# Optimization experiments

Measured on AMD Instinct MI355X. Metric: run time of the kernel, lower is better.

## Reference

```python
import jax, jax.numpy as jnp
import numpy as np

B, S, H, E = 32, 4096, 512, 512

def setup_inputs() -> dict:
    key = jax.random.key(0)
    ks = jax.random.split(key, 11)
    sc = 1.0 / np.sqrt(H)
    return {
        "context": jax.random.normal(ks[0], (B, S, H), jnp.float32),
        "h": jax.random.normal(ks[1], (B, H), jnp.float32),
        "x": jax.random.normal(ks[2], (B, E), jnp.float32),
        "We": jax.random.normal(ks[3], (H, H), jnp.float32) * sc,
        "be": jax.random.normal(ks[4], (H,), jnp.float32) * sc,
        "Wd": jax.random.normal(ks[5], (H, H), jnp.float32) * sc,
        "bd": jax.random.normal(ks[6], (H,), jnp.float32) * sc,
        "Wv": jax.random.normal(ks[7], (H,), jnp.float32) * sc,
        "bv": jax.random.normal(ks[8], (1,), jnp.float32) * sc,
        "Wr": jax.random.normal(ks[9], (2 * H, 2 * H + E), jnp.float32) * (1.0 / np.sqrt(2 * H + E)),
        "br": jax.random.normal(ks[10], (2 * H,), jnp.float32) * sc,
    }

def reference(context, h, x, We, be, Wd, bd, Wv, bv, Wr, br):
    # gamma_encoder: [B,S,H]; gamma_decoder: [B,1,H]
    ge = jnp.einsum('bsh,kh->bsk', context, We) + be
    gd = h @ Wd.T + bd
    # additive scores -> [B,S]
    scores = jnp.einsum('bsh,h->bs', jnp.tanh(ge + gd[:, None, :]), Wv) + bv[0]
    weights = jax.nn.softmax(scores, axis=1)
    # context vector c_t: [B,H]
    c_t = jnp.einsum('bs,bsh->bh', weights, context)
    # linear_r on [c_t, h, x] -> [B,2H]
    r_t = jnp.concatenate([c_t, h, x], axis=1) @ Wr.T + br
    # maxout over pairs: view [B,H,2].max(-1)
    output = jnp.max(r_t.reshape(-1, r_t.shape[1] // 2, 2), axis=2)
    return (output, weights)
```

## Files before the change

### kernel.cpp

```cpp
#include <hip/hip_runtime.h>

typedef __attribute__((ext_vector_type(8))) short bf16x8;
typedef __attribute__((ext_vector_type(16))) float f32x16;

typedef __attribute__((address_space(3))) unsigned int lds_u32;
typedef __attribute__((address_space(1))) unsigned int glb_u32;

__device__ inline unsigned int cvt_pk_bf16(float lo, float hi){
  unsigned int r;
  asm("v_cvt_pk_bf16_f32 %0, %1, %2" : "=v"(r) : "v"(lo), "v"(hi));
  return r;
}
__device__ inline bf16x8 pack8(float4 a, float4 b){
  union { unsigned int u[4]; bf16x8 v; } r;
  r.u[0]=cvt_pk_bf16(a.x,a.y); r.u[1]=cvt_pk_bf16(a.z,a.w);
  r.u[2]=cvt_pk_bf16(b.x,b.y); r.u[3]=cvt_pk_bf16(b.z,b.w);
  return r.v;
}
__device__ inline float fast_tanh(float x){
  float e = __builtin_amdgcn_exp2f(x * 2.8853900817779268f);
  return 1.0f - 2.0f * __builtin_amdgcn_rcpf(e + 1.0f);
}
#define LOG2E 1.4426950408889634f

__global__ __launch_bounds__(256) void we_conv(const float* __restrict__ We,
                                               uint4* __restrict__ weFrag){
  int gid = blockIdx.x * 256 + threadIdx.x;
  int l  = gid & 63;
  int hc = gid >> 10;
  int colv = (hc >> 1)*32 + (l & 31);
  int k = ((hc & 1) << 8) + ((gid >> 6) & 15)*16 + (l >> 5)*8;
  const float4* src = (const float4*)(We + colv*512 + k);
  float4 f0 = src[0], f1 = src[1];
  weFrag[gid] = make_uint4(cvt_pk_bf16(f0.x,f0.y), cvt_pk_bf16(f0.z,f0.w),
                           cvt_pk_bf16(f1.x,f1.y), cvt_pk_bf16(f1.z,f1.w));
}

__global__ __launch_bounds__(256) void gd_kernel(const float* __restrict__ hvec,
                                                 const float* __restrict__ Wd,
                                                 const float* __restrict__ bd,
                                                 const float* __restrict__ be,
                                                 float* __restrict__ gd){
  __shared__ float hs[512];
  int b = blockIdx.x >> 2, kc = blockIdx.x & 3;
  int tid = threadIdx.x;
  hs[tid]       = hvec[b*512 + tid];
  hs[tid + 256] = hvec[b*512 + 256 + tid];
  __syncthreads();
  int k  = kc*128 + (tid >> 1);
  int hh = (tid & 1) * 256;
  const float4* wrow = (const float4*)(Wd + (size_t)k*512 + hh);
  const float4* hv4  = (const float4*)(hs + hh);
  float acc = 0.f;
  #pragma unroll 8
  for (int i = 0; i < 64; ++i){
    float4 w = wrow[i]; float4 u = hv4[i];
    acc += w.x*u.x + w.y*u.y + w.z*u.z + w.w*u.w;
  }
  acc += __shfl_xor(acc, 1);
  if ((tid & 1) == 0) gd[b*512 + k] = acc + bd[k] + be[k];
}

__global__ __launch_bounds__(256, 2) void score_kernel(
    const float* __restrict__ ctx, const char* __restrict__ weFrag,
    const float* __restrict__ gd, const float* __restrict__ Wv,
    float* __restrict__ scores, unsigned int* __restrict__ ctp,
    float* __restrict__ MS){
  __shared__ char lds[3*16384 + 4096];
  float* gdwv = (float*)(lds + 49152);

  const int tid  = threadIdx.x;
  const int wid  = tid >> 6;
  const int lane = tid & 63;
  const int bid  = blockIdx.x;
  const int row0 = bid * 128;
  const int b    = bid >> 5;
  const int col  = lane & 31;
  const int hi   = lane >> 5;

  if (tid < 128) ((float4*)gdwv)[tid] = ((const float4*)(gd + b*512))[tid];
  else           ((float4*)gdwv)[tid] = ((const float4*)Wv)[tid - 128];

  bf16x8 afrag[32];
  {
    const float4* ap = (const float4*)(ctx + (size_t)(row0 + wid*32 + col)*512 + hi*8);
    #pragma unroll
    for (int t = 0; t < 32; ++t)
      afrag[t] = pack8(ap[t*4], ap[t*4 + 1]);
  }

  asm volatile("s_waitcnt lgkmcnt(0)" ::: "memory");

  #define ISSUE(HC, BUF) do { \
    const char* _g = weFrag + ((size_t)(HC))*16384 + wid*4096; \
    char* _l = lds + (BUF)*16384 + wid*4096; \
    _Pragma("unroll") \
    for (int _i = 0; _i < 4; ++_i) \
      __builtin_amdgcn_global_load_lds((const glb_u32*)(_g + _i*1024 + lane*16), \
                                       (lds_u32*)(_l + _i*1024), 16, 0, 0); \
  } while(0)

  ISSUE(0, 0);
  ISSUE(1, 1);

  f32x16 acc;
  float sc[16];
  #pragma unroll
  for (int r = 0; r < 16; ++r) sc[r] = 0.f;

  for (int nc = 0; nc < 16; ++nc){
    const int hc0 = 2*nc, hc1 = 2*nc + 1;

    asm volatile("s_waitcnt vmcnt(4)" ::: "memory");
    __builtin_amdgcn_s_barrier();
    if (hc0 < 30) ISSUE(hc0 + 2, (hc0 + 2) % 3);
    {
      const char* bb = lds + (hc0 % 3)*16384 + lane*16;
      #pragma unroll
      for (int r = 0; r < 16; ++r) acc[r] = 0.f;
      __builtin_amdgcn_s_setprio(1);
      #pragma unroll
      for (int t = 0; t < 16; ++t){
        bf16x8 bf = *(const bf16x8*)(bb + t*1024);
        acc = __builtin_amdgcn_mfma_f32_32x32x16_bf16(afrag[t], bf, acc, 0, 0, 0);
      }
      __builtin_amdgcn_s_setprio(0);
    }

    if (nc < 15) asm volatile("s_waitcnt vmcnt(4)" ::: "memory");
    else         asm volatile("s_waitcnt vmcnt(0)" ::: "memory");
    __builtin_amdgcn_s_barrier();
    if (hc1 < 30) ISSUE(hc1 + 2, (hc1 + 2) % 3);
    {
      const char* bb = lds + (hc1 % 3)*16384 + lane*16;
      __builtin_amdgcn_s_setprio(1);
      #pragma unroll
      for (int t = 0; t < 16; ++t){
        bf16x8 bf = *(const bf16x8*)(bb + t*1024);
        acc = __builtin_amdgcn_mfma_f32_32x32x16_bf16(afrag[16 + t], bf, acc, 0, 0, 0);
      }
      __builtin_amdgcn_s_setprio(0);
    }

    {
      float gdv = gdwv[nc*32 + col];
      float wvv = gdwv[512 + nc*32 + col];
      #pragma unroll
      for (int r = 0; r < 16; ++r)
        sc[r] += fast_tanh(acc[r] + gdv) * wvv;
    }
  }
  #undef ISSUE

  #pragma unroll
  for (int r = 0; r < 16; ++r){
    #pragma unroll
    for (int m = 1; m <= 16; m <<= 1) sc[r] += __shfl_xor(sc[r], m);
  }

  float* scl  = gdwv;
  float* wl   = gdwv + 128;
  float* redp = gdwv + 256;
  __syncthreads();

  if (col == 0){
    int rbase = wid*32 + 4*hi;
    float* so = scores + row0 + rbase;
    #pragma unroll
    for (int r = 0; r < 16; ++r){
      int rr = (r & 3) + 8*(r >> 2);
      so[rr] = sc[r];
      scl[rbase + rr] = sc[r];
    }
  }
  __syncthreads();

  float M = -1e30f;
  {
    const float4* s4 = (const float4*)scl;
    #pragma unroll
    for (int i = 0; i < 32; ++i){
      float4 v = s4[i];
      M = fmaxf(M, fmaxf(fmaxf(v.x, v.y), fmaxf(v.z, v.w)));
    }
  }
  if (tid < 128){
    float w = __builtin_amdgcn_exp2f((scl[tid] - M) * LOG2E);
    wl[tid] = w;
    #pragma unroll
    for (int o = 1; o < 64; o <<= 1) w += __shfl_xor(w, o);
    if ((tid & 63) == 0) redp[tid >> 6] = w;
  }
  __syncthreads();
  float S_blk = redp[0] + redp[1];

  float cA = 0.f, cB = 0.f;
  #pragma unroll
  for (int p = 0; p < 4; ++p){
    if (wid == p){
      int rl = col;
      char* dst = lds + rl*1024;
      int swz = (rl & 7) << 4;
      #pragma unroll
      for (int t = 0; t < 32; ++t){
        union { bf16x8 v; uint4 q; } u; u.v = afrag[t];
        *(uint4*)(dst + ((t*32 + hi*16) ^ swz)) = u.q;
      }
    }
    __syncthreads();
    const float* wp = wl + p*32;
    #pragma unroll 8
    for (int r = 0; r < 32; ++r){
      unsigned int u = *(const unsigned int*)(lds + r*1024 + ((tid*4) ^ ((r & 7) << 4)));
      float cw = wp[r];
      union { unsigned int q; float f; } flo, fhi;
      flo.q = u << 16;
      fhi.q = u & 0xffff0000u;
      cA += cw * flo.f;
      cB += cw * fhi.f;
    }
    __syncthreads();
  }
  ctp[(size_t)bid*256 + tid] = cvt_pk_bf16(cA, cB);
  if (tid == 0){ MS[2*bid] = M; MS[2*bid + 1] = S_blk; }
}

__global__ __launch_bounds__(256) void combine_kernel(const unsigned int* __restrict__ ctp,
                                                      const float* __restrict__ MS,
                                                      float* __restrict__ ct,
                                                      float* __restrict__ mbuf){
  __shared__ float wsh[32];
  __shared__ float msh[2];
  int b = blockIdx.x, tid = threadIdx.x;
  if (tid < 32){
    float Mi = MS[(b*32 + tid)*2];
    float Si = MS[(b*32 + tid)*2 + 1];
    float M = Mi;
    #pragma unroll
    for (int o = 1; o < 32; o <<= 1) M = fmaxf(M, __shfl_xor(M, o));
    float w = __builtin_amdgcn_exp2f((Mi - M) * LOG2E);
    float d = w * Si;
    #pragma unroll
    for (int o = 1; o < 32; o <<= 1) d += __shfl_xor(d, o);
    wsh[tid] = w;
    if (tid == 0){ msh[0] = M; msh[1] = 1.0f / d; }
  }
  __syncthreads();
  float invd = msh[1];
  float a0 = 0.f, a1 = 0.f;
  #pragma unroll 8
  for (int i = 0; i < 32; ++i){
    unsigned int u = ctp[(size_t)(b*32 + i)*256 + tid];
    float w = wsh[i];
    union { unsigned int q; float f; } flo, fhi;
    flo.q = u << 16;
    fhi.q = u & 0xffff0000u;
    a0 += w * flo.f;
    a1 += w * fhi.f;
  }
  ((float2*)(ct + b*512))[tid] = make_float2(a0 * invd, a1 * invd);
  if (tid == 0){ mbuf[2*b] = msh[0]; mbuf[2*b + 1] = invd; }
}

__global__ __launch_bounds__(256) void weights_kernel(const float* __restrict__ scores,
                                                      const float* __restrict__ mbuf,
                                                      float* __restrict__ weights){
  int b = blockIdx.x, tid = threadIdx.x;
  float M = mbuf[2*b], invd = mbuf[2*b + 1];
  const float4* src = (const float4*)(scores + b*4096);
  float4* dst = (float4*)(weights + b*4096);
  #pragma unroll
  for (int i = 0; i < 4; ++i){
    float4 v = src[tid + i*256];
    v.x = __builtin_amdgcn_exp2f((v.x - M) * LOG2E) * invd;
    v.y = __builtin_amdgcn_exp2f((v.y - M) * LOG2E) * invd;
    v.z = __builtin_amdgcn_exp2f((v.z - M) * LOG2E) * invd;
    v.w = __builtin_amdgcn_exp2f((v.w - M) * LOG2E) * invd;
    dst[tid + i*256] = v;
  }
}

__global__ __launch_bounds__(256) void final_kernel(
    const float* __restrict__ ct, const float* __restrict__ hvec,
    const float* __restrict__ x, const float* __restrict__ Wr,
    const float* __restrict__ br, float* __restrict__ out){
  __shared__ float xs[8][1536];
  int bt = blockIdx.x >> 4;
  int it = blockIdx.x & 15;
  int tid = threadIdx.x;
  int b0 = bt * 8;
  for (int idx = tid; idx < 8*1536; idx += 256){
    int bl = idx / 1536, j = idx % 1536;
    int b = b0 + bl;
    float v = (j < 512) ? ct[b*512 + j]
            : (j < 1024) ? hvec[b*512 + (j - 512)]
            : x[b*512 + (j - 1024)];
    xs[bl][j] = v;
  }
  __syncthreads();
  int i = it*64 + (tid & 63);
  int bl0 = (tid >> 6) * 2;
  const float4* wrow = (const float4*)(Wr + (size_t)i*1536);
  const float4* x0 = (const float4*)xs[bl0];
  const float4* x1 = (const float4*)xs[bl0 + 1];
  float a0 = 0.f, a1 = 0.f;
  #pragma unroll 4
  for (int k = 0; k < 384; ++k){
    float4 w = wrow[k];
    float4 u0 = x0[k], u1 = x1[k];
    a0 += w.x*u0.x + w.y*u0.y + w.z*u0.z + w.w*u0.w;
    a1 += w.x*u1.x + w.y*u1.y + w.z*u1.z + w.w*u1.w;
  }
  float bias = br[i];
  a0 += bias; a1 += bias;
  float n0 = __shfl_xor(a0, 1);
  float n1 = __shfl_xor(a1, 1);
  if ((tid & 1) == 0){
    out[(b0 + bl0    )*512 + (i >> 1)] = fmaxf(a0, n0);
    out[(b0 + bl0 + 1)*512 + (i >> 1)] = fmaxf(a1, n1);
  }
}

extern "C" void kernel_launch(void* const* d_in, const int* in_sizes, int n_in,
                              void* d_out, int out_size, void* d_ws, size_t ws_size,
                              hipStream_t stream){
  const float* ctx  = (const float*)d_in[0];
  const float* hvec = (const float*)d_in[1];
  const float* x    = (const float*)d_in[2];
  const float* We   = (const float*)d_in[3];
  const float* be   = (const float*)d_in[4];
  const float* Wd   = (const float*)d_in[5];
  const float* bd   = (const float*)d_in[6];
  const float* Wv   = (const float*)d_in[7];
  const float* Wr   = (const float*)d_in[9];
  const float* br   = (const float*)d_in[10];

  float* out     = (float*)d_out;
  float* weights = out + 32*512;

  char* ws = (char*)d_ws;
  char* weFrag   = ws;
  float* scores  = (float*)(ws + (512 << 10));
  unsigned int* ctp = (unsigned int*)(ws + (1024 << 10));
  float* MS      = (float*)(ws + (2 << 20));
  float* mbuf    = (float*)(ws + (2 << 20) + (16 << 10));
  float* ct      = (float*)(ws + (2 << 20) + (32 << 10));
  float* gd      = (float*)(ws + (2 << 20) + (96 << 10));

  we_conv<<<128, 256, 0, stream>>>(We, (uint4*)weFrag);
  gd_kernel<<<128, 256, 0, stream>>>(hvec, Wd, bd, be, gd);
  score_kernel<<<1024, 256, 0, stream>>>(ctx, weFrag, gd, Wv, scores, ctp, MS);
  combine_kernel<<<32, 256, 0, stream>>>(ctp, MS, ct, mbuf);
  weights_kernel<<<32, 256, 0, stream>>>(scores, mbuf, weights);
  final_kernel<<<64, 256, 0, stream>>>(ct, hvec, x, Wr, br, out);
}
```

Measured before the change: 190.6 us.

## Halve We staging chunks to cut LDS and raise occupancy to four blocks

Splits each 16KB We fragment chunk into two 8KB quarter-chunks, triple-buffered in LDS, so LDS per block falls from about 52KB to 40KB. The launch bound is raised from 2 to 4 blocks per SM. Score scratch buffers move to dedicated LDS regions rather than reusing the gd/Wv area. The goal is more resident waves to hide load latency, at the cost of twice as many barriers and waitcnts, and register pressure capped by the higher bound (afrag alone takes 128 VGPRs).

```diff
diff --git a/kernel.cpp b/kernel.cpp
--- a/kernel.cpp
+++ b/kernel.cpp
@@ -61,13 +61,16 @@
   if ((tid & 1) == 0) gd[b*512 + k] = acc + bd[k] + be[k];
 }
 
-__global__ __launch_bounds__(256, 2) void score_kernel(
+__global__ __launch_bounds__(256, 4) void score_kernel(
     const float* __restrict__ ctx, const char* __restrict__ weFrag,
     const float* __restrict__ gd, const float* __restrict__ Wv,
     float* __restrict__ scores, unsigned int* __restrict__ ctp,
     float* __restrict__ MS){
-  __shared__ char lds[3*16384 + 4096];
-  float* gdwv = (float*)(lds + 49152);
+  __shared__ char lds[40960];
+  float* gdwv = (float*)(lds + 24576);
+  float* scl  = (float*)(lds + 32768);
+  float* wl   = (float*)(lds + 33280);
+  float* redp = (float*)(lds + 33792);
 
   const int tid  = threadIdx.x;
   const int wid  = tid >> 6;
@@ -91,17 +94,17 @@
 
   asm volatile("s_waitcnt lgkmcnt(0)" ::: "memory");
 
-  #define ISSUE(HC, BUF) do { \
-    const char* _g = weFrag + ((size_t)(HC))*16384 + wid*4096; \
-    char* _l = lds + (BUF)*16384 + wid*4096; \
-    _Pragma("unroll") \
-    for (int _i = 0; _i < 4; ++_i) \
-      __builtin_amdgcn_global_load_lds((const glb_u32*)(_g + _i*1024 + lane*16), \
-                                       (lds_u32*)(_l + _i*1024), 16, 0, 0); \
+  #define ISSUE_Q(QC) do { \
+    const char* _g = weFrag + ((size_t)((QC) >> 1))*16384 + ((QC) & 1)*8192 \
+                     + wid*2048 + lane*16; \
+    char* _l = lds + ((QC) % 3)*8192 + wid*2048; \
+    __builtin_amdgcn_global_load_lds((const glb_u32*)_g, (lds_u32*)_l, 16, 0, 0); \
+    __builtin_amdgcn_global_load_lds((const glb_u32*)(_g + 1024), \
+                                     (lds_u32*)(_l + 1024), 16, 0, 0); \
   } while(0)
 
-  ISSUE(0, 0);
-  ISSUE(1, 1);
+  ISSUE_Q(0);
+  ISSUE_Q(1);
 
   f32x16 acc;
   float sc[16];
@@ -109,48 +112,35 @@
   for (int r = 0; r < 16; ++r) sc[r] = 0.f;
 
   for (int nc = 0; nc < 16; ++nc){
-    const int hc0 = 2*nc, hc1 = 2*nc + 1;
-
-    asm volatile("s_waitcnt vmcnt(4)" ::: "memory");
-    __builtin_amdgcn_s_barrier();
-    if (hc0 < 30) ISSUE(hc0 + 2, (hc0 + 2) % 3);
-    {
-      const char* bb = lds + (hc0 % 3)*16384 + lane*16;
-      #pragma unroll
-      for (int r = 0; r < 16; ++r) acc[r] = 0.f;
-      __builtin_amdgcn_s_setprio(1);
-      #pragma unroll
-      for (int t = 0; t < 16; ++t){
-        bf16x8 bf = *(const bf16x8*)(bb + t*1024);
-        acc = __builtin_amdgcn_mfma_f32_32x32x16_bf16(afrag[t], bf, acc, 0, 0, 0);
+    #pragma unroll
+    for (int r = 0; r < 16; ++r) acc[r] = 0.f;
+
+    #pragma unroll
+    for (int j = 0; j < 4; ++j){
+      const int qc = nc*4 + j;
+      if (qc < 63) asm volatile("s_waitcnt vmcnt(2)" ::: "memory");
+      else         asm volatile("s_waitcnt vmcnt(0)" ::: "memory");
+      __builtin_amdgcn_s_barrier();
+      if (qc < 62) ISSUE_Q(qc + 2);
+      {
+        const char* bb = lds + (qc % 3)*8192 + lane*16;
+        __builtin_amdgcn_s_setprio(1);
+        #pragma unroll
+        for (int t = 0; t < 8; ++t){
+          bf16x8 bf = *(const bf16x8*)(bb + t*1024);
+          acc = __builtin_amdgcn_mfma_f32_32x32x16_bf16(afrag[j*8 + t], bf, acc, 0, 0, 0);
+        }
+        __builtin_amdgcn_s_setprio(0);
       }
-      __builtin_amdgcn_s_setprio(0);
-    }
-
-    if (nc < 15) asm volatile("s_waitcnt vmcnt(4)" ::: "memory");
-    else         asm volatile("s_waitcnt vmcnt(0)" ::: "memory");
-    __builtin_amdgcn_s_barrier();
-    if (hc1 < 30) ISSUE(hc1 + 2, (hc1 + 2) % 3);
-    {
-      const char* bb = lds + (hc1 % 3)*16384 + lane*16;
-      __builtin_amdgcn_s_setprio(1);
-      #pragma unroll
-      for (int t = 0; t < 16; ++t){
-        bf16x8 bf = *(const bf16x8*)(bb + t*1024);
-        acc = __builtin_amdgcn_mfma_f32_32x32x16_bf16(afrag[16 + t], bf, acc, 0, 0, 0);
-      }
-      __builtin_amdgcn_s_setprio(0);
-    }
-
-    {
-      float gdv = gdwv[nc*32 + col];
-      float wvv = gdwv[512 + nc*32 + col];
-      #pragma unroll
-      for (int r = 0; r < 16; ++r)
-        sc[r] += fast_tanh(acc[r] + gdv) * wvv;
-    }
-  }
-  #undef ISSUE
+    }
+
+    float gdv = gdwv[nc*32 + col];
+    float wvv = gdwv[512 + nc*32 + col];
+    #pragma unroll
+    for (int r = 0; r < 16; ++r)
+      sc[r] += fast_tanh(acc[r] + gdv) * wvv;
+  }
+  #undef ISSUE_Q
 
   #pragma unroll
   for (int r = 0; r < 16; ++r){
@@ -158,11 +148,7 @@
     for (int m = 1; m <= 16; m <<= 1) sc[r] += __shfl_xor(sc[r], m);
   }
 
-  float* scl  = gdwv;
-  float* wl   = gdwv + 128;
-  float* redp = gdwv + 256;
-  __syncthreads();
-
+  __syncthreads();
   if (col == 0){
     int rbase = wid*32 + 4*hi;
     float* so = scores + row0 + rbase;
```

New measurement: 321.8 us. 68.9% more time.
